# Performance work log

Hardware: AMD Instinct MI355X
Metric: run time of the kernel (lower is better)

Reference implementation:

```python
import jax, jax.numpy as jnp
import numpy as np

EPS_NORM = 1e-12  # F.normalize eps
EPS_LN = 1e-5     # LayerNorm eps
TEMP = 0.1


def _l2norm(v, axis=-1):
    n = jnp.linalg.norm(v, axis=axis, keepdims=True)
    return v / jnp.maximum(n, EPS_NORM)


def setup_inputs() -> dict:
    key = jax.random.key(0)
    ks = jax.random.split(key, 6)
    B, D, P = 65536, 1024, 32
    x = jax.random.normal(ks[0], (B, D), dtype=jnp.float32)
    Wi = jax.random.normal(ks[1], (D, D), dtype=jnp.float32) * 0.02
    bi = jnp.zeros((D,), dtype=jnp.float32)
    Wo = jax.random.normal(ks[2], (D, 2 * D), dtype=jnp.float32) * 0.02
    bo = jnp.zeros((D,), dtype=jnp.float32)
    gamma = jnp.ones((D,), dtype=jnp.float32)
    beta = jnp.zeros((D,), dtype=jnp.float32)
    prototypes = _l2norm(jax.random.normal(ks[3], (P, D), dtype=jnp.float32))
    return {"x": x, "Wi": Wi, "bi": bi, "Wo": Wo, "bo": bo,
            "gamma": gamma, "beta": beta, "prototypes": prototypes}


def reference(x, Wi, bi, Wo, bo, gamma, beta, prototypes):
    # h = in_proj(x)
    h = x @ Wi.T + bi                      # [B, D]
    h_norm = _l2norm(h)
    proto_norm = _l2norm(prototypes)       # [P, D]
    sim = (h_norm @ proto_norm.T) / TEMP   # [B, P]
    attn = jax.nn.softmax(sim, axis=-1)
    retrieved = attn @ prototypes          # [B, D]
    combined = jnp.concatenate([x, retrieved], axis=-1)  # [B, 2D]
    out = jax.nn.gelu(combined @ Wo.T + bo, approximate=False)
    # dropout is identity in eval mode
    y = out + x
    mu = jnp.mean(y, axis=-1, keepdims=True)
    var = jnp.var(y, axis=-1, keepdims=True)
    return (y - mu) * jax.lax.rsqrt(var + EPS_LN) * gamma + beta
```

## Files before the change

kernel.cpp:

```cpp
#include <hip/hip_runtime.h>
#include <hip/hip_bf16.h>
#include <math.h>

typedef unsigned short u16;
typedef __attribute__((ext_vector_type(8))) short bf16x8;
typedef __attribute__((ext_vector_type(4))) float f32x4;
typedef __attribute__((address_space(1))) unsigned int gu32;
typedef __attribute__((address_space(3))) unsigned int lu32;

#define DD 1024
#define PP 32

__device__ __forceinline__ u16 f2bf(float f) {
  unsigned u = __float_as_uint(f);
  unsigned r = u + 0x7fffu + ((u >> 16) & 1u);
  return (u16)(r >> 16);
}
__device__ __forceinline__ float bf2f(u16 h) {
  return __uint_as_float(((unsigned)h) << 16);
}

__device__ __forceinline__ float gelu_t(float v) {
  float u = v + 0.044715f * v * v * v;
  float p = __builtin_amdgcn_exp2f(2.302590614f * u);
  float th = 1.0f - 2.0f * __builtin_amdgcn_rcpf(p + 1.0f);
  return 0.5f * v * (1.0f + th);
}

__global__ __launch_bounds__(256) void k_convert(const float* __restrict__ in,
                                                 u16* __restrict__ out, int n4) {
  for (int i = blockIdx.x * 256 + threadIdx.x; i < n4; i += gridDim.x * 256) {
    float4 v = ((const float4*)in)[i];
    ushort4 o;
    o.x = f2bf(v.x); o.y = f2bf(v.y); o.z = f2bf(v.z); o.w = f2bf(v.w);
    ((ushort4*)out)[i] = o;
  }
}

__global__ __launch_bounds__(256) void k_convert_wo(const float* __restrict__ Wo,
                                                    u16* __restrict__ WoB) {
  int i = blockIdx.x * 256 + threadIdx.x;
  int n = i >> 8, c4 = i & 255;
  float4 v = ((const float4*)(Wo + (size_t)n * 2048))[c4];
  ushort4 o;
  o.x = f2bf(v.x); o.y = f2bf(v.y); o.z = f2bf(v.z); o.w = f2bf(v.w);
  *(ushort4*)(WoB + (size_t)n * 1088 + c4 * 4) = o;
}

__global__ __launch_bounds__(256) void k_proto_prep(const float* __restrict__ protos,
                                                    u16* __restrict__ pb) {
  __shared__ float sb[4];
  int row = blockIdx.x, tid = threadIdx.x;
  float4 v = ((const float4*)(protos + row * DD))[tid];
  float q = v.x * v.x + v.y * v.y + v.z * v.z + v.w * v.w;
#pragma unroll
  for (int off = 32; off; off >>= 1) q += __shfl_xor(q, off);
  if ((tid & 63) == 0) sb[tid >> 6] = q;
  __syncthreads();
  q = sb[0] + sb[1] + sb[2] + sb[3];
  float inv = 1.0f / fmaxf(sqrtf(q), 1e-12f);
  ushort4 o;
  o.x = f2bf(v.x * inv); o.y = f2bf(v.y * inv); o.z = f2bf(v.z * inv); o.w = f2bf(v.w * inv);
  ((ushort4*)(pb + row * DD))[tid] = o;
}

__global__ __launch_bounds__(256) void k_p2(const float* __restrict__ Wo,
                                            const float* __restrict__ protos,
                                            u16* __restrict__ WoB) {
  __shared__ float swo[1024];
  int n = blockIdx.x, tid = threadIdx.x;
  ((float4*)swo)[tid] = ((const float4*)(Wo + (size_t)n * 2048 + 1024))[tid];
  __syncthreads();
  int w = tid >> 6, lane = tid & 63;
#pragma unroll
  for (int q = 0; q < 8; ++q) {
    int p = w * 8 + q;
    const float* pr = protos + (size_t)p * 1024 + lane * 16;
    const float* wv = swo + lane * 16;
    float d = 0.f;
#pragma unroll
    for (int j = 0; j < 16; ++j) d += wv[j] * pr[j];
#pragma unroll
    for (int off = 32; off; off >>= 1) d += __shfl_xor(d, off);
    if (lane == 0) WoB[(size_t)n * 1088 + 1024 + p] = f2bf(d);
  }
  if (tid < 32) WoB[(size_t)n * 1088 + 1056 + tid] = 0;
}

#define GLL(gsrc, ldst) __builtin_amdgcn_global_load_lds((gu32*)(gsrc), (lu32*)(ldst), 16, 0, 0)

template <int EPI, int NT>
__global__ __launch_bounds__(512, 2) void k_gemmF(const u16* __restrict__ A,
                                                  const u16* __restrict__ Aext,
                                                  const u16* __restrict__ Bm, int bstride,
                                                  const float* __restrict__ bias,
                                                  const u16* __restrict__ residb,
                                                  u16* __restrict__ Cout,
                                                  int nbn) {
  __shared__ u16 Lsh[65536];
#define ALS(bufv, idx) (Lsh + (bufv) * 16384 + (idx))
#define BLS(bufv, idx) (Lsh + 32768 + (bufv) * 16384 + (idx))
  const int tid = threadIdx.x;
  const int wid = tid >> 6, lane = tid & 63;
  const int wm = wid >> 2, wn = wid & 3;
  const int lm = lane & 15, lk = lane >> 4;

  const int scol_sw = (((lane & 7) ^ ((lane >> 3) & 7)) << 3);
  const int srow = lane >> 3;

  int g = blockIdx.x;
  int cpx = gridDim.x >> 3;
  int lin = (g & 7) * cpx + (g >> 3);
  int bn = lin % nbn, bm = lin / nbn;
  const size_t bmBase = (size_t)bm * 256;
  const size_t bnBase = (size_t)bn * 256;

  f32x4 acc[8][4];
#pragma unroll
  for (int i = 0; i < 8; ++i)
#pragma unroll
    for (int j = 0; j < 4; ++j) acc[i][j] = (f32x4){0.f, 0.f, 0.f, 0.f};

  bf16x8 a[4][2], b0[2][2], b1[2][2];

#define STAGE_A(bufv, kt, mh) do {                                              \
    int arow = (mh) * 64 + wid * 8 + srow;                                      \
    const u16 *ap0, *ap1;                                                       \
    if ((kt) < 16) {                                                            \
      ap0 = A + (bmBase + arow) * (size_t)1024 + scol_sw + (kt) * 64;           \
      ap1 = A + (bmBase + 128 + arow) * (size_t)1024 + scol_sw + (kt) * 64;     \
    } else {                                                                    \
      ap0 = Aext + (bmBase + arow) * (size_t)64 + scol_sw;                      \
      ap1 = Aext + (bmBase + 128 + arow) * (size_t)64 + scol_sw;                \
    }                                                                           \
    GLL(ap0, ALS(bufv, ((mh) * 64 + wid * 8) * 64));                            \
    GLL(ap1, ALS(bufv, (128 + (mh) * 64 + wid * 8) * 64));                      \
  } while (0)

#define STAGE_B(bufv, kt, nh) do {                                              \
    int br0 = ((wid >> 2) << 6) + (nh) * 32 + ((wid & 3) << 3);                 \
    int bcol = scol_sw + (kt) * 64;                                             \
    GLL(Bm + (bnBase + br0 + srow) * (size_t)bstride + bcol, BLS(bufv, br0 * 64)); \
    GLL(Bm + (bnBase + 128 + br0 + srow) * (size_t)bstride + bcol, BLS(bufv, (128 + br0) * 64)); \
  } while (0)

#define LOAD_A(bufv, mh) do {                                                   \
    _Pragma("unroll") for (int mi2 = 0; mi2 < 4; ++mi2) {                       \
      int row = wm * 128 + (mh) * 64 + mi2 * 16 + lm;                           \
      _Pragma("unroll") for (int kk = 0; kk < 2; ++kk)                          \
        a[mi2][kk] = *(const bf16x8*)ALS(bufv, row * 64 + ((kk * 32 + lk * 8) ^ ((lm & 7) << 3))); \
    }                                                                           \
  } while (0)

#define LOAD_B(dst, bufv, nh) do {                                              \
    _Pragma("unroll") for (int ni2 = 0; ni2 < 2; ++ni2) {                       \
      int row = wn * 64 + (nh) * 32 + ni2 * 16 + lm;                            \
      _Pragma("unroll") for (int kk = 0; kk < 2; ++kk)                          \
        dst[ni2][kk] = *(const bf16x8*)BLS(bufv, row * 64 + ((kk * 32 + lk * 8) ^ ((lm & 7) << 3))); \
    }                                                                           \
  } while (0)

#define BARRIER do { __builtin_amdgcn_s_barrier(); asm volatile("" ::: "memory"); } while (0)

#define MFMA_Q(bb, mh, nh) do {                                                 \
    __builtin_amdgcn_s_setprio(1);                                              \
    _Pragma("unroll") for (int mi2 = 0; mi2 < 4; ++mi2)                         \
    _Pragma("unroll") for (int ni2 = 0; ni2 < 2; ++ni2)                         \
    _Pragma("unroll") for (int kk = 0; kk < 2; ++kk)                            \
      acc[(mh) * 4 + mi2][(nh) * 2 + ni2] = __builtin_amdgcn_mfma_f32_16x16x32_bf16( \
          a[mi2][kk], bb[ni2][kk], acc[(mh) * 4 + mi2][(nh) * 2 + ni2], 0, 0, 0); \
    __builtin_amdgcn_s_setprio(0);                                              \
  } while (0)

#define TILE(T, P) do {                                                         \
    asm volatile("s_waitcnt vmcnt(0)" ::: "memory");                            \
    BARRIER;                                                                    \
    if ((T) + 1 < NT) {                                                         \
      STAGE_A((P) ^ 1, (T) + 1, 0); STAGE_B((P) ^ 1, (T) + 1, 0);               \
      STAGE_A((P) ^ 1, (T) + 1, 1); STAGE_B((P) ^ 1, (T) + 1, 1);               \
    }                                                                           \
    LOAD_A(P, 0); LOAD_B(b0, P, 0);                                             \
    MFMA_Q(b0, 0, 0);                                                           \
    LOAD_B(b1, P, 1);                                                           \
    MFMA_Q(b1, 0, 1);                                                           \
    LOAD_A(P, 1);                                                               \
    MFMA_Q(b1, 1, 1);                                                           \
    MFMA_Q(b0, 1, 0);                                                           \
  } while (0)

  STAGE_A(0, 0, 0); STAGE_B(0, 0, 0); STAGE_A(0, 0, 1); STAGE_B(0, 0, 1);

#pragma unroll
  for (int T = 0; T + 1 < NT; T += 2) {
    TILE(T, 0);
    TILE(T + 1, 1);
  }
  if (NT & 1) TILE(NT - 1, 0);

  __syncthreads();
  u16* eb = Lsh + wid * 4608;
  const size_t gr0 = bmBase + wm * 128;
  const int gc0 = (int)bnBase + wn * 64;
#pragma unroll
  for (int ch = 0; ch < 2; ++ch) {
#pragma unroll
    for (int mi2 = 0; mi2 < 4; ++mi2) {
      int mi = ch * 4 + mi2;
#pragma unroll
      for (int ni = 0; ni < 4; ++ni) {
        int col = ni * 16 + lm;
        float bv = bias[gc0 + ni * 16 + lm];
#pragma unroll
        for (int r = 0; r < 4; ++r) {
          int rowL = mi2 * 16 + lk * 4 + r;
          float v = acc[mi][ni][r] + bv;
          if (EPI == 1) v = gelu_t(v);
          eb[rowL * 72 + (col ^ (((rowL >> 2) & 3) << 3))] = f2bf(v);
        }
      }
    }
#pragma unroll
    for (int i = 0; i < 8; ++i) {
      int rowL = i * 8 + (lane >> 3);
      int c8 = (lane & 7) * 8;
      bf16x8 yv = *(const bf16x8*)&eb[rowL * 72 + (c8 ^ (((rowL >> 2) & 3) << 3))];
      size_t grow = gr0 + ch * 64 + rowL;
      if (EPI == 0) {
        *(bf16x8*)(Cout + grow * 1024 + gc0 + c8) = yv;
      } else {
        bf16x8 rv = *(const bf16x8*)(residb + grow * 1024 + gc0 + c8);
        bf16x8 ov;
#pragma unroll
        for (int j = 0; j < 8; ++j)
          ov[j] = (short)f2bf(bf2f((u16)yv[j]) + bf2f((u16)rv[j]));
        *(bf16x8*)(Cout + grow * 2048 + gc0 + c8) = ov;
      }
    }
  }
#undef STAGE_A
#undef STAGE_B
#undef LOAD_A
#undef LOAD_B
#undef MFMA_Q
#undef TILE
#undef BARRIER
#undef ALS
#undef BLS
}

__global__ __launch_bounds__(256) void k_mid2(const u16* __restrict__ h,
                                              const u16* __restrict__ pb,
                                              u16* __restrict__ ab) {
  __shared__ u16 attn_sm[4][16 * 32];
  const int tid = threadIdx.x;
  const int w = tid >> 6, lane = tid & 63;
  const int lm = lane & 15, lk = lane >> 4;
  const int row0 = blockIdx.x * 64 + w * 16;

  f32x4 zero = {0.f, 0.f, 0.f, 0.f};
  f32x4 acc0 = zero, acc1 = zero;
  float ss = 0.f;

  const u16* hrow = h + ((size_t)(row0 + lm) << 10) + lk * 8;
  const u16* pb0 = pb + (size_t)lm * DD + lk * 8;
  const u16* pb1 = pb + (size_t)(16 + lm) * DD + lk * 8;
#pragma unroll 4
  for (int k0 = 0; k0 < DD; k0 += 32) {
    bf16x8 af = *(const bf16x8*)(hrow + k0);
    bf16x8 b0 = *(const bf16x8*)(pb0 + k0);
    bf16x8 b1 = *(const bf16x8*)(pb1 + k0);
    acc0 = __builtin_amdgcn_mfma_f32_16x16x32_bf16(af, b0, acc0, 0, 0, 0);
    acc1 = __builtin_amdgcn_mfma_f32_16x16x32_bf16(af, b1, acc1, 0, 0, 0);
#pragma unroll
    for (int j = 0; j < 8; ++j) {
      float hv = bf2f((u16)af[j]);
      ss += hv * hv;
    }
  }
  ss += __shfl_xor(ss, 16);
  ss += __shfl_xor(ss, 32);
  float inv = 10.0f / fmaxf(sqrtf(ss), 1e-12f);

  float a0[4], a1[4];
#pragma unroll
  for (int r = 0; r < 4; ++r) {
    float invr = __shfl(inv, lk * 4 + r);
    float s0 = acc0[r] * invr;
    float s1 = acc1[r] * invr;
    float mr = fmaxf(s0, s1);
#pragma unroll
    for (int off = 1; off < 16; off <<= 1) mr = fmaxf(mr, __shfl_xor(mr, off));
    float e0 = expf(s0 - mr);
    float e1 = expf(s1 - mr);
    float sum = e0 + e1;
#pragma unroll
    for (int off = 1; off < 16; off <<= 1) sum += __shfl_xor(sum, off);
    float rs = 1.0f / sum;
    a0[r] = e0 * rs;
    a1[r] = e1 * rs;
  }

  u16* as = attn_sm[w];
#pragma unroll
  for (int r = 0; r < 4; ++r) {
    as[(lk * 4 + r) * 32 + lm] = f2bf(a0[r]);
    as[(lk * 4 + r) * 32 + 16 + lm] = f2bf(a1[r]);
  }
  __syncthreads();
  int rr = lane >> 2, c8 = (lane & 3) << 3;
  int4 v = *(const int4*)(as + rr * 32 + c8);
  size_t orow = (size_t)(row0 + rr) * 64;
  *(int4*)(ab + orow + c8) = v;
  int4 z = {0, 0, 0, 0};
  *(int4*)(ab + orow + 32 + c8) = z;
}

__global__ __launch_bounds__(256) void k_ln2(u16* __restrict__ ybase,
                                             float* __restrict__ out,
                                             const float* __restrict__ gamma,
                                             const float* __restrict__ beta) {
  __shared__ float sb[8];
  size_t row = blockIdx.x;
  int tid = threadIdx.x;
  ushort4 v4 = ((const ushort4*)(ybase + row * 2048))[tid];
  float y0 = bf2f(v4.x), y1 = bf2f(v4.y), y2 = bf2f(v4.z), y3 = bf2f(v4.w);
  float s = y0 + y1 + y2 + y3;
  float q = y0 * y0 + y1 * y1 + y2 * y2 + y3 * y3;
#pragma unroll
  for (int off = 32; off; off >>= 1) { s += __shfl_xor(s, off); q += __shfl_xor(q, off); }
  if ((tid & 63) == 0) { sb[tid >> 6] = s; sb[4 + (tid >> 6)] = q; }
  __syncthreads();
  s = sb[0] + sb[1] + sb[2] + sb[3];
  q = sb[4] + sb[5] + sb[6] + sb[7];
  float mu = s * (1.f / 1024.f);
  float var = q * (1.f / 1024.f) - mu * mu;
  float rstd = rsqrtf(var + 1e-5f);
  float4 g = ((const float4*)gamma)[tid];
  float4 b = ((const float4*)beta)[tid];
  float4 o;
  o.x = (y0 - mu) * rstd * g.x + b.x;
  o.y = (y1 - mu) * rstd * g.y + b.y;
  o.z = (y2 - mu) * rstd * g.z + b.z;
  o.w = (y3 - mu) * rstd * g.w + b.w;
  ((float4*)(out + (row << 10)))[tid] = o;
}

extern "C" void kernel_launch(void* const* d_in, const int* in_sizes, int n_in,
                              void* d_out, int out_size, void* d_ws, size_t ws_size,
                              hipStream_t stream) {
  const float* x      = (const float*)d_in[0];
  const float* Wi     = (const float*)d_in[1];
  const float* bi     = (const float*)d_in[2];
  const float* Wo     = (const float*)d_in[3];
  const float* bo     = (const float*)d_in[4];
  const float* gamma  = (const float*)d_in[5];
  const float* beta   = (const float*)d_in[6];
  const float* protos = (const float*)d_in[7];
  const int Brows = in_sizes[0] / DD;

  u16* xb   = (u16*)d_ws;
  u16* WiB  = xb + (size_t)Brows * 1024;
  u16* WoB  = WiB + (size_t)1024 * 1024;
  u16* pb   = WoB + (size_t)1024 * 1088;
  u16* ab   = pb + (size_t)PP * DD;
  u16* hbuf = (u16*)d_out;
  u16* ybuf = (u16*)d_out;

  k_convert<<<4096, 256, 0, stream>>>(x, xb, Brows * 256);
  k_convert<<<1024, 256, 0, stream>>>(Wi, WiB, 1024 * 1024 / 4);
  k_convert_wo<<<1024, 256, 0, stream>>>(Wo, WoB);
  k_proto_prep<<<PP, 256, 0, stream>>>(protos, pb);
  k_p2<<<1024, 256, 0, stream>>>(Wo, protos, WoB);

  const int nbn = 1024 / 256;
  const int nwg = nbn * (Brows / 256);

  k_gemmF<0, 16><<<nwg, 512, 0, stream>>>(xb, xb, WiB, 1024, bi, nullptr,
                                          hbuf, nbn);
  k_mid2<<<Brows / 64, 256, 0, stream>>>(hbuf, pb, ab);
  k_gemmF<1, 17><<<nwg, 512, 0, stream>>>(xb, ab, WoB, 1088, bo, xb,
                                          ybuf, nbn);
  k_ln2<<<Brows, 256, 0, stream>>>(ybuf, (float*)d_out, gamma, beta);
}
```

Measured before the change: 524.7 us.

## Fuse prototype similarity and row norms into first GEMM epilogue

The first GEMM's epilogue now computes partial dot products of each h tile against the normalized prototypes using MFMA, plus partial sums of squares per row. It writes these fp32 partials to workspace, so the full h matrix is never stored. A lightweight softmax kernel then reduces the partials across column blocks and produces the attention weights. This removes the write and re-read of the bf16 h matrix (B×1024) and the separate similarity GEMM pass. In exchange the epilogue does extra work and LDS traffic, and writes fp32 partial buffers of B×128 and B×16.

```diff
diff --git a/kernel.cpp b/kernel.cpp
--- a/kernel.cpp
+++ b/kernel.cpp
@@ -96,7 +96,10 @@
                                                   const float* __restrict__ bias,
                                                   const u16* __restrict__ residb,
                                                   u16* __restrict__ Cout,
-                                                  int nbn) {
+                                                  int nbn,
+                                                  const u16* __restrict__ pbn,
+                                                  float* __restrict__ simp,
+                                                  float* __restrict__ ssp) {
   __shared__ u16 Lsh[65536];
 #define ALS(bufv, idx) (Lsh + (bufv) * 16384 + (idx))
 #define BLS(bufv, idx) (Lsh + 32768 + (bufv) * 16384 + (idx))
@@ -201,33 +204,101 @@
   u16* eb = Lsh + wid * 4608;
   const size_t gr0 = bmBase + wm * 128;
   const int gc0 = (int)bnBase + wn * 64;
-#pragma unroll
-  for (int ch = 0; ch < 2; ++ch) {
-#pragma unroll
-    for (int mi2 = 0; mi2 < 4; ++mi2) {
-      int mi = ch * 4 + mi2;
-#pragma unroll
-      for (int ni = 0; ni < 4; ++ni) {
-        int col = ni * 16 + lm;
-        float bv = bias[gc0 + ni * 16 + lm];
-#pragma unroll
-        for (int r = 0; r < 4; ++r) {
-          int rowL = mi2 * 16 + lk * 4 + r;
-          float v = acc[mi][ni][r] + bv;
-          if (EPI == 1) v = gelu_t(v);
-          eb[rowL * 72 + (col ^ (((rowL >> 2) & 3) << 3))] = f2bf(v);
+
+  if (EPI == 2) {
+    bf16x8 bp[2][2];
+#pragma unroll
+    for (int ph = 0; ph < 2; ++ph)
+#pragma unroll
+      for (int kk = 0; kk < 2; ++kk)
+        bp[ph][kk] = *(const bf16x8*)(pbn + (size_t)(ph * 16 + lm) * 1024 + gc0 + kk * 32 + lk * 8);
+    f32x4 sa[2][4][2];
+#pragma unroll
+    for (int ch = 0; ch < 2; ++ch) {
+#pragma unroll
+      for (int mi2 = 0; mi2 < 4; ++mi2) {
+        int mi = ch * 4 + mi2;
+#pragma unroll
+        for (int ni = 0; ni < 4; ++ni) {
+          int col = ni * 16 + lm;
+          float bv = bias[gc0 + ni * 16 + lm];
+#pragma unroll
+          for (int r = 0; r < 4; ++r) {
+            int rowL = mi2 * 16 + lk * 4 + r;
+            eb[rowL * 72 + (col ^ (((rowL >> 2) & 3) << 3))] = f2bf(acc[mi][ni][r] + bv);
+          }
         }
       }
+#pragma unroll
+      for (int rg = 0; rg < 4; ++rg) {
+        int rowL = rg * 16 + lm;
+        int swz = ((lm >> 2) & 3) << 3;
+        bf16x8 af0 = *(const bf16x8*)&eb[rowL * 72 + ((lk * 8) ^ swz)];
+        bf16x8 af1 = *(const bf16x8*)&eb[rowL * 72 + ((32 + lk * 8) ^ swz)];
+        float sq = 0.f;
+#pragma unroll
+        for (int j = 0; j < 8; ++j) {
+          float h0 = bf2f((u16)af0[j]), h1 = bf2f((u16)af1[j]);
+          sq += h0 * h0 + h1 * h1;
+        }
+        sq += __shfl_xor(sq, 16);
+        sq += __shfl_xor(sq, 32);
+        if (lk == 0)
+          ssp[(gr0 + ch * 64 + rg * 16 + lm) * 16 + bn * 4 + wn] = sq;
+        f32x4 z = {0.f, 0.f, 0.f, 0.f};
+        f32x4 s0 = __builtin_amdgcn_mfma_f32_16x16x32_bf16(af0, bp[0][0], z, 0, 0, 0);
+        s0 = __builtin_amdgcn_mfma_f32_16x16x32_bf16(af1, bp[0][1], s0, 0, 0, 0);
+        f32x4 s1 = __builtin_amdgcn_mfma_f32_16x16x32_bf16(af0, bp[1][0], z, 0, 0, 0);
+        s1 = __builtin_amdgcn_mfma_f32_16x16x32_bf16(af1, bp[1][1], s1, 0, 0, 0);
+        sa[ch][rg][0] = s0;
+        sa[ch][rg][1] = s1;
+      }
     }
-#pragma unroll
-    for (int i = 0; i < 8; ++i) {
-      int rowL = i * 8 + (lane >> 3);
-      int c8 = (lane & 7) * 8;
-      bf16x8 yv = *(const bf16x8*)&eb[rowL * 72 + (c8 ^ (((rowL >> 2) & 3) << 3))];
-      size_t grow = gr0 + ch * 64 + rowL;
-      if (EPI == 0) {
-        *(bf16x8*)(Cout + grow * 1024 + gc0 + c8) = yv;
-      } else {
+    __syncthreads();
+    float* part = (float*)Lsh;
+#pragma unroll
+    for (int ch = 0; ch < 2; ++ch)
+#pragma unroll
+      for (int rg = 0; rg < 4; ++rg)
+#pragma unroll
+        for (int ph = 0; ph < 2; ++ph)
+#pragma unroll
+          for (int r = 0; r < 4; ++r) {
+            int row = wm * 128 + ch * 64 + rg * 16 + lk * 4 + r;
+            part[wn * 8192 + row * 32 + ph * 16 + lm] = sa[ch][rg][ph][r];
+          }
+    __syncthreads();
+    for (int i = tid; i < 8192; i += 512) {
+      int row = i >> 5, p = i & 31;
+      float s = part[row * 32 + p] + part[8192 + row * 32 + p] +
+                part[16384 + row * 32 + p] + part[24576 + row * 32 + p];
+      simp[(bmBase + row) * 128 + (size_t)bn * 32 + p] = s;
+    }
+  } else {
+#pragma unroll
+    for (int ch = 0; ch < 2; ++ch) {
+#pragma unroll
+      for (int mi2 = 0; mi2 < 4; ++mi2) {
+        int mi = ch * 4 + mi2;
+#pragma unroll
+        for (int ni = 0; ni < 4; ++ni) {
+          int col = ni * 16 + lm;
+          float bv = bias[gc0 + ni * 16 + lm];
+#pragma unroll
+          for (int r = 0; r < 4; ++r) {
+            int rowL = mi2 * 16 + lk * 4 + r;
+            float v = acc[mi][ni][r] + bv;
+            v = gelu_t(v);
+            eb[rowL * 72 + (col ^ (((rowL >> 2) & 3) << 3))] = f2bf(v);
+          }
+        }
+      }
+#pragma unroll
+      for (int i = 0; i < 8; ++i) {
+        int rowL = i * 8 + (lane >> 3);
+        int c8 = (lane & 7) * 8;
+        bf16x8 yv = *(const bf16x8*)&eb[rowL * 72 + (c8 ^ (((rowL >> 2) & 3) << 3))];
+        size_t grow = gr0 + ch * 64 + rowL;
         bf16x8 rv = *(const bf16x8*)(residb + grow * 1024 + gc0 + c8);
         bf16x8 ov;
 #pragma unroll
@@ -248,71 +319,33 @@
 #undef BLS
 }
 
-__global__ __launch_bounds__(256) void k_mid2(const u16* __restrict__ h,
-                                              const u16* __restrict__ pb,
+__global__ __launch_bounds__(256) void k_soft(const float* __restrict__ simp,
+                                              const float* __restrict__ ssp,
                                               u16* __restrict__ ab) {
-  __shared__ u16 attn_sm[4][16 * 32];
-  const int tid = threadIdx.x;
-  const int w = tid >> 6, lane = tid & 63;
-  const int lm = lane & 15, lk = lane >> 4;
-  const int row0 = blockIdx.x * 64 + w * 16;
-
-  f32x4 zero = {0.f, 0.f, 0.f, 0.f};
-  f32x4 acc0 = zero, acc1 = zero;
-  float ss = 0.f;
-
-  const u16* hrow = h + ((size_t)(row0 + lm) << 10) + lk * 8;
-  const u16* pb0 = pb + (size_t)lm * DD + lk * 8;
-  const u16* pb1 = pb + (size_t)(16 + lm) * DD + lk * 8;
-#pragma unroll 4
-  for (int k0 = 0; k0 < DD; k0 += 32) {
-    bf16x8 af = *(const bf16x8*)(hrow + k0);
-    bf16x8 b0 = *(const bf16x8*)(pb0 + k0);
-    bf16x8 b1 = *(const bf16x8*)(pb1 + k0);
-    acc0 = __builtin_amdgcn_mfma_f32_16x16x32_bf16(af, b0, acc0, 0, 0, 0);
-    acc1 = __builtin_amdgcn_mfma_f32_16x16x32_bf16(af, b1, acc1, 0, 0, 0);
-#pragma unroll
-    for (int j = 0; j < 8; ++j) {
-      float hv = bf2f((u16)af[j]);
-      ss += hv * hv;
-    }
+  const int wv = threadIdx.x >> 6, lane = threadIdx.x & 63;
+  int rowBase = blockIdx.x * 32 + wv * 8;
+#pragma unroll
+  for (int i = 0; i < 8; ++i) {
+    int row = rowBase + i;
+    const float* sp = simp + (size_t)row * 128;
+    float v = sp[lane] + sp[64 + lane];
+    v += __shfl_xor(v, 32);
+    float ssv = (lane < 16) ? ssp[(size_t)row * 16 + lane] : 0.f;
+    ssv += __shfl_xor(ssv, 1); ssv += __shfl_xor(ssv, 2);
+    ssv += __shfl_xor(ssv, 4); ssv += __shfl_xor(ssv, 8);
+    float ss = __shfl(ssv, 0);
+    float inv = 10.0f / fmaxf(sqrtf(ss), 1e-12f);
+    float s = v * inv;
+    float m = s;
+#pragma unroll
+    for (int off = 1; off < 32; off <<= 1) m = fmaxf(m, __shfl_xor(m, off));
+    float e = expf(s - m);
+    float sum = e;
+#pragma unroll
+    for (int off = 1; off < 32; off <<= 1) sum += __shfl_xor(sum, off);
+    float a = e / sum;
+    ab[(size_t)row * 64 + lane] = (lane < 32) ? f2bf(a) : (u16)0;
   }
-  ss += __shfl_xor(ss, 16);
-  ss += __shfl_xor(ss, 32);
-  float inv = 10.0f / fmaxf(sqrtf(ss), 1e-12f);
-
-  float a0[4], a1[4];
-#pragma unroll
-  for (int r = 0; r < 4; ++r) {
-    float invr = __shfl(inv, lk * 4 + r);
-    float s0 = acc0[r] * invr;
-    float s1 = acc1[r] * invr;
-    float mr = fmaxf(s0, s1);
-#pragma unroll
-    for (int off = 1; off < 16; off <<= 1) mr = fmaxf(mr, __shfl_xor(mr, off));
-    float e0 = expf(s0 - mr);
-    float e1 = expf(s1 - mr);
-    float sum = e0 + e1;
-#pragma unroll
-    for (int off = 1; off < 16; off <<= 1) sum += __shfl_xor(sum, off);
-    float rs = 1.0f / sum;
-    a0[r] = e0 * rs;
-    a1[r] = e1 * rs;
-  }
-
-  u16* as = attn_sm[w];
-#pragma unroll
-  for (int r = 0; r < 4; ++r) {
-    as[(lk * 4 + r) * 32 + lm] = f2bf(a0[r]);
-    as[(lk * 4 + r) * 32 + 16 + lm] = f2bf(a1[r]);
-  }
-  __syncthreads();
-  int rr = lane >> 2, c8 = (lane & 3) << 3;
-  int4 v = *(const int4*)(as + rr * 32 + c8);
-  size_t orow = (size_t)(row0 + rr) * 64;
-  *(int4*)(ab + orow + c8) = v;
-  int4 z = {0, 0, 0, 0};
-  *(int4*)(ab + orow + 32 + c8) = z;
 }
 
 __global__ __launch_bounds__(256) void k_ln2(u16* __restrict__ ybase,
@@ -363,7 +396,8 @@
   u16* WoB  = WiB + (size_t)1024 * 1024;
   u16* pb   = WoB + (size_t)1024 * 1088;
   u16* ab   = pb + (size_t)PP * DD;
-  u16* hbuf = (u16*)d_out;
+  float* simp = (float*)(ab + (size_t)Brows * 64);
+  float* ssp  = simp + (size_t)Brows * 128;
   u16* ybuf = (u16*)d_out;
 
   k_convert<<<4096, 256, 0, stream>>>(x, xb, Brows * 256);
@@ -375,10 +409,10 @@
   const int nbn = 1024 / 256;
   const int nwg = nbn * (Brows / 256);
 
-  k_gemmF<0, 16><<<nwg, 512, 0, stream>>>(xb, xb, WiB, 1024, bi, nullptr,
-                                          hbuf, nbn);
-  k_mid2<<<Brows / 64, 256, 0, stream>>>(hbuf, pb, ab);
+  k_gemmF<2, 16><<<nwg, 512, 0, stream>>>(xb, xb, WiB, 1024, bi, nullptr,
+                                          nullptr, nbn, pb, simp, ssp);
+  k_soft<<<Brows / 32, 256, 0, stream>>>(simp, ssp, ab);
   k_gemmF<1, 17><<<nwg, 512, 0, stream>>>(xb, ab, WoB, 1088, bo, xb,
-                                          ybuf, nbn);
+                                          ybuf, nbn, nullptr, nullptr, nullptr);
   k_ln2<<<Brows, 256, 0, stream>>>(ybuf, (float*)d_out, gamma, beta);
 }
```

Measured after the change: 493.3 us. 1.06x faster.
